# Kernel tuning notes

Hardware: AMD Instinct MI355X
Metric: run time of the kernel (lower is better)

## Reference

```python
import jax, jax.numpy as jnp
import numpy as np

N_ATOMS = 393216   # 4096 molecules * ~96 atoms
N_FEAT = 128
NB_FILTER = 128
NB_AFFINE = 11     # max_deg(10) + 1 - min_deg(0)
BATCH = 4096


def setup_inputs() -> dict:
    key = jax.random.key(0)
    k1, k2, k3, k4 = jax.random.split(key, 4)
    atoms = jax.random.normal(k1, (N_ATOMS, N_FEAT), jnp.float32)
    # stacked per-degree affine weights (glorot-ish scale)
    W = jax.random.normal(k2, (NB_AFFINE, N_FEAT, NB_FILTER), jnp.float32) / jnp.sqrt(jnp.float32(N_FEAT))
    b = jax.random.normal(k3, (NB_AFFINE, NB_FILTER), jnp.float32) * 0.01
    # contiguous degree layout: deg_slice[k] = (start, count), atoms sorted by degree
    counts = np.full(NB_AFFINE, N_ATOMS // NB_AFFINE, dtype=np.int32)
    counts[-1] += N_ATOMS - counts.sum()
    starts = np.concatenate([[0], np.cumsum(counts)[:-1]]).astype(np.int32)
    deg_slice = jnp.asarray(np.stack([starts, counts], axis=1))  # (11, 2) int32
    membership = jax.random.randint(k4, (N_ATOMS,), 0, BATCH, dtype=jnp.int32)
    return {"atoms": atoms, "W": W, "b": b, "deg_slice": deg_slice,
            "membership": membership, "batch_size": BATCH}


def reference(atoms, W, b, deg_slice, membership, batch_size):
    # atoms: (N, F); W: (K, F, O); b: (K, O); deg_slice: (K, 2)
    n = atoms.shape[0]
    nb_affine = W.shape[0]
    # Per-atom degree index from contiguous deg_slice layout:
    # deg_idx[i] = number of degree blocks that end at or before atom i.
    ends = jnp.cumsum(deg_slice[:, 1])                     # (K,)
    idx = jnp.arange(n, dtype=ends.dtype)
    deg_idx = jnp.sum(idx[:, None] >= ends[None, :], axis=1)  # (N,)
    # Per-degree affine: each atom uses the (W, b) of its degree block.
    out = jnp.zeros((n, W.shape[2]), dtype=atoms.dtype)
    for k in range(nb_affine):  # fixed small structural loop (11 distinct weight sets)
        yk = atoms @ W[k] + b[k]
        out = out + jnp.where((deg_idx == k)[:, None], yk, jnp.zeros((), atoms.dtype))
    # graph_gather: dynamic_partition + per-partition reduce_sum + concat == segment_sum
    pooled = jax.ops.segment_sum(out, membership, num_segments=batch_size)  # (B, O)
    # activation is 'linear' (identity); dropout is None
    return pooled
```

## Files before the change

### kernel.cpp

```cpp
#include <hip/hip_runtime.h>
#include <hip/hip_bf16.h>


typedef short bf16x8 __attribute__((ext_vector_type(8)));
typedef float f32x4  __attribute__((ext_vector_type(4)));

__device__ __forceinline__ unsigned short f2bf(float f) {
    unsigned int u = __builtin_bit_cast(unsigned int, f);
    u += 0x7fffu + ((u >> 16) & 1u);
    return (unsigned short)(u >> 16);
}

__device__ __forceinline__ int deg_of(int i, const int* __restrict__ ds, int K) {
    int k = 0, end = 0;
    for (int kk = 0; kk < K; ++kk) { end += ds[2 * kk + 1]; k += (i >= end) ? 1 : 0; }
    return k;
}

__global__ __launch_bounds__(256) void k_hist(
    const int* __restrict__ mem, const int* __restrict__ ds,
    unsigned* __restrict__ hist, int N, int K)
{
    int i = blockIdx.x * 256 + threadIdx.x;
    if (i >= N) return;
    int key = mem[i] * K + deg_of(i, ds, K);
    atomicAdd(&hist[key], 1u);
}

__global__ __launch_bounds__(1024) void k_scan(
    const unsigned* __restrict__ hist, unsigned* __restrict__ binstart, int B, int K)
{
    __shared__ unsigned segsum[4096];
    __shared__ unsigned aux[1024];
    int t = threadIdx.x;
    int CH = (B + 1023) >> 10;
    unsigned loc = 0;
    for (int j = 0; j < CH; ++j) {
        int s = t * CH + j;
        unsigned tot = 0;
        if (s < B) {
            for (int k = 0; k < K; ++k) tot += hist[s * K + k];
            segsum[s] = tot;
        }
        loc += tot;
    }
    aux[t] = loc;
    __syncthreads();
    for (int d = 1; d < 1024; d <<= 1) {
        unsigned v = (t >= d) ? aux[t - d] : 0u;
        __syncthreads();
        aux[t] += v;
        __syncthreads();
    }
    unsigned run = (t > 0) ? aux[t - 1] : 0u;
    for (int j = 0; j < CH; ++j) {
        int s = t * CH + j;
        if (s < B) {
            unsigned b2 = run;
            for (int k = 0; k < K; ++k) { binstart[s * K + k] = b2; b2 += hist[s * K + k]; }
            run = b2;
        }
    }
    if (t == 1023) binstart[(size_t)B * K] = run;
}

__global__ __launch_bounds__(256) void k_scatter(
    const int* __restrict__ mem, const int* __restrict__ ds,
    const unsigned* __restrict__ binstart, unsigned* __restrict__ cursor,
    unsigned* __restrict__ idx, int N, int K)
{
    int i = blockIdx.x * 256 + threadIdx.x;
    if (i >= N) return;
    int key = mem[i] * K + deg_of(i, ds, K);
    unsigned p = atomicAdd(&cursor[key], 1u);
    idx[binstart[key] + p] = (unsigned)i;
}

__global__ __launch_bounds__(256) void k_wconv(
    const float* __restrict__ W, unsigned short* __restrict__ Wb)
{
    __shared__ unsigned short t[128 * 130];
    int k = blockIdx.x;
    const float* Wk = W + (size_t)k * 16384;
    unsigned short* Wbk = Wb + (size_t)k * 16384;
    for (int e = threadIdx.x; e < 16384; e += 256) {
        int f = e >> 7, c = e & 127;
        t[f * 130 + c] = f2bf(Wk[e]);
    }
    __syncthreads();
    for (int e = threadIdx.x; e < 16384; e += 256) {
        int c = e >> 7, f = e & 127;
        Wbk[e] = t[f * 130 + c];
    }
}

__global__ __launch_bounds__(128) void k_phaseA(
    const float* __restrict__ atoms, const float* __restrict__ bias,
    const unsigned* __restrict__ binstart, const unsigned* __restrict__ idx,
    unsigned short* __restrict__ S, float* __restrict__ bsum, int K)
{
    int s = blockIdx.x, f = threadIdx.x;
    float bs = 0.f;
    for (int k = 0; k < K; ++k) {
        unsigned st = binstart[s * K + k];
        unsigned en = binstart[s * K + k + 1];
        float a0 = 0.f, a1 = 0.f, a2 = 0.f, a3 = 0.f;
        unsigned j = st;
        for (; j + 4 <= en; j += 4) {
            unsigned r0 = idx[j], r1 = idx[j + 1], r2 = idx[j + 2], r3 = idx[j + 3];
            a0 += atoms[(size_t)r0 * 128 + f];
            a1 += atoms[(size_t)r1 * 128 + f];
            a2 += atoms[(size_t)r2 * 128 + f];
            a3 += atoms[(size_t)r3 * 128 + f];
        }
        for (; j < en; ++j) a0 += atoms[(size_t)idx[j] * 128 + f];
        float acc = (a0 + a1) + (a2 + a3);
        S[(size_t)(s * K + k) * 128 + f] = f2bf(acc);
        bs += (float)(en - st) * bias[k * 128 + f];
    }
    bsum[(size_t)s * 128 + f] = bs;
}

__global__ __launch_bounds__(64) void k_phaseB(
    const unsigned short* __restrict__ S,
    const unsigned short* __restrict__ Wb,
    const float* __restrict__ bsum,
    float* __restrict__ out,
    int K)
{
    int bx   = blockIdx.x;
    int s0   = (bx >> 2) * 16;
    int c0   = (bx & 3) * 32;
    int lane = threadIdx.x;
    int quad = lane >> 4, cb = lane & 15;

    const int KD = K * 128;
    f32x4 acc0 = (f32x4){0.f, 0.f, 0.f, 0.f};
    f32x4 acc1 = (f32x4){0.f, 0.f, 0.f, 0.f};

    const unsigned short* Arow = S  + (size_t)(s0 + cb) * KD + quad * 8;
    const unsigned short* B0   = Wb + (size_t)(c0 + cb)      * 128 + quad * 8;
    const unsigned short* B1   = Wb + (size_t)(c0 + 16 + cb) * 128 + quad * 8;

    #pragma unroll 1
    for (int kk = 0; kk < K; ++kk) {
        #pragma unroll
        for (int k0 = 0; k0 < 128; k0 += 32) {
            bf16x8 a  = *reinterpret_cast<const bf16x8*>(Arow + kk * 128 + k0);
            bf16x8 b0 = *reinterpret_cast<const bf16x8*>(B0 + (size_t)kk * 16384 + k0);
            bf16x8 b1 = *reinterpret_cast<const bf16x8*>(B1 + (size_t)kk * 16384 + k0);
            acc0 = __builtin_amdgcn_mfma_f32_16x16x32_bf16(a, b0, acc0, 0, 0, 0);
            acc1 = __builtin_amdgcn_mfma_f32_16x16x32_bf16(a, b1, acc1, 0, 0, 0);
        }
    }
    #pragma unroll
    for (int reg = 0; reg < 4; ++reg) {
        int s = s0 + quad * 4 + reg;
        int c = c0 + cb;
        out[(size_t)s * 128 + c]      = acc0[reg] + bsum[(size_t)s * 128 + c];
        out[(size_t)s * 128 + c + 16] = acc1[reg] + bsum[(size_t)s * 128 + c + 16];
    }
}

#define TM 64
#define LDA 136
#define LDW 136
__global__ __launch_bounds__(256, 2) void degree_affine_pool(
    const float* __restrict__ atoms, const float* __restrict__ W,
    const float* __restrict__ bias, const int* __restrict__ deg_slice,
    const int* __restrict__ membership, float* __restrict__ out, int K)
{
    __shared__ unsigned short Alds[TM * LDA];
    __shared__ unsigned short Wlds[128 * LDW];
    const int bid = blockIdx.x, tid = threadIdx.x;
    int k = -1, tile = 0, acc_t = 0;
    for (int kk = 0; kk < K; ++kk) {
        int c = deg_slice[2 * kk + 1];
        int nt = (c + TM - 1) >> 6;
        if (k < 0 && bid < acc_t + nt) { k = kk; tile = bid - acc_t; }
        acc_t += nt;
    }
    if (k < 0) return;
    const int start = deg_slice[2 * k], cnt = deg_slice[2 * k + 1];
    const int row0 = start + tile * TM;
    const int rows_valid = min(TM, cnt - tile * TM);
    for (int e = tid; e < TM * 32; e += 256) {
        int r = e >> 5, f4 = e & 31;
        float4 v = make_float4(0.f, 0.f, 0.f, 0.f);
        if (r < rows_valid)
            v = *reinterpret_cast<const float4*>(atoms + (size_t)(row0 + r) * 128 + f4 * 4);
        unsigned lo = (unsigned)f2bf(v.x) | ((unsigned)f2bf(v.y) << 16);
        unsigned hi = (unsigned)f2bf(v.z) | ((unsigned)f2bf(v.w) << 16);
        *reinterpret_cast<uint2*>(&Alds[r * LDA + f4 * 4]) = make_uint2(lo, hi);
    }
    const float* Wk = W + (size_t)k * 16384;
    for (int e = tid; e < 8192; e += 256) {
        int c = e & 127, f2 = e >> 7;
        unsigned p = (unsigned)f2bf(Wk[(2 * f2) * 128 + c]) |
                     ((unsigned)f2bf(Wk[(2 * f2 + 1) * 128 + c]) << 16);
        *reinterpret_cast<unsigned*>(&Wlds[c * LDW + 2 * f2]) = p;
    }
    __syncthreads();
    const int wave = tid >> 6, lane = tid & 63, quad = lane >> 4, cb = lane & 15;
    f32x4 acc[8];
    #pragma unroll
    for (int ct = 0; ct < 8; ++ct) acc[ct] = (f32x4){0.f, 0.f, 0.f, 0.f};
    #pragma unroll
    for (int k0 = 0; k0 < 128; k0 += 32) {
        bf16x8 af = *reinterpret_cast<const bf16x8*>(&Alds[(wave * 16 + cb) * LDA + k0 + quad * 8]);
        #pragma unroll
        for (int ct = 0; ct < 8; ++ct) {
            bf16x8 bf = *reinterpret_cast<const bf16x8*>(&Wlds[(ct * 16 + cb) * LDW + k0 + quad * 8]);
            acc[ct] = __builtin_amdgcn_mfma_f32_16x16x32_bf16(af, bf, acc[ct], 0, 0, 0);
        }
    }
    int segs[4]; bool valid[4];
    #pragma unroll
    for (int reg = 0; reg < 4; ++reg) {
        int rl = wave * 16 + quad * 4 + reg;
        valid[reg] = (rl < rows_valid);
        segs[reg] = valid[reg] ? membership[row0 + rl] : 0;
    }
    const float* bk = bias + k * 128;
    #pragma unroll
    for (int ct = 0; ct < 8; ++ct) {
        int col = ct * 16 + cb;
        float bv = bk[col];
        #pragma unroll
        for (int reg = 0; reg < 4; ++reg)
            if (valid[reg])
                __hip_atomic_fetch_add(out + (size_t)segs[reg] * 128 + col,
                                       acc[ct][reg] + bv, __ATOMIC_RELAXED,
                                       __HIP_MEMORY_SCOPE_AGENT);
    }
}

static inline size_t aln(size_t x) { return (x + 255) & ~(size_t)255; }

extern "C" void kernel_launch(void* const* d_in, const int* in_sizes, int n_in,
                              void* d_out, int out_size, void* d_ws, size_t ws_size,
                              hipStream_t stream) {
    const float* atoms = (const float*)d_in[0];
    const float* W     = (const float*)d_in[1];
    const float* bias  = (const float*)d_in[2];
    const int*   deg   = (const int*)d_in[3];
    const int*   mem   = (const int*)d_in[4];
    float*       out   = (float*)d_out;

    const int K = in_sizes[3] / 2;
    const int N = in_sizes[0] / 128;
    const int B = out_size / 128;

    size_t oWb   = 0;                         size_t sWb   = (size_t)K * 16384 * 2;
    size_t oHist = aln(oWb + sWb);            size_t sHist = (size_t)B * K * 4;
    size_t oCur  = oHist + sHist;             size_t sCur  = sHist;
    size_t oBin  = aln(oCur + sCur);          size_t sBin  = ((size_t)B * K + 1) * 4;
    size_t oIdx  = aln(oBin + sBin);          size_t sIdx  = (size_t)N * 4;
    size_t oBsum = aln(oIdx + sIdx);          size_t sBsum = (size_t)B * 128 * 4;
    size_t oS    = aln(oBsum + sBsum);        size_t sS    = (size_t)B * K * 128 * 2;
    size_t total = oS + sS;

    if (ws_size < total || B > 4096) {
        (void)hipMemsetAsync(d_out, 0, (size_t)out_size * sizeof(float), stream);
        const int blocks = (N + TM - 1) / TM + K;
        degree_affine_pool<<<blocks, 256, 0, stream>>>(atoms, W, bias, deg, mem, out, K);
        return;
    }

    char* ws = (char*)d_ws;
    unsigned short* Wb   = (unsigned short*)(ws + oWb);
    unsigned*       hist = (unsigned*)(ws + oHist);
    unsigned*       cur  = (unsigned*)(ws + oCur);
    unsigned*       bin  = (unsigned*)(ws + oBin);
    unsigned*       idx  = (unsigned*)(ws + oIdx);
    float*          bsum = (float*)(ws + oBsum);
    unsigned short* S    = (unsigned short*)(ws + oS);

    (void)hipMemsetAsync(hist, 0, sHist + sCur, stream);

    const int nb = (N + 255) / 256;
    k_hist   <<<nb, 256, 0, stream>>>(mem, deg, hist, N, K);
    k_scan   <<<1, 1024, 0, stream>>>(hist, bin, B, K);
    k_scatter<<<nb, 256, 0, stream>>>(mem, deg, bin, cur, idx, N, K);
    k_wconv  <<<K, 256, 0, stream>>>(W, Wb);
    k_phaseA <<<B, 128, 0, stream>>>(atoms, bias, bin, idx, S, bsum, K);
    k_phaseB <<<(B / 16) * 4, 64, 0, stream>>>(S, Wb, bsum, out, K);
}
```

Baseline: 423.6 us.

## Fuse weight conversion into scan, drop cursor buffer, parallelize gather per bin

Merges the bf16 weight conversion into the scan launch as extra blocks, removing one kernel launch. The scatter now increments the bin start array directly, so after scatter it holds bin ends, which removes the separate cursor buffer and half of the memset. Phase A now gives each block two (segment, degree) bins instead of one segment with a serial loop over degrees, which exposes K times more blocks and uses 8-way unrolled gathers. The bias sum moves into the phase B epilogue, computed from bin counts. The trade-off is redundant bias loops in phase B and a tighter fallback condition.

```diff
diff --git a/kernel.cpp b/kernel.cpp
--- a/kernel.cpp
+++ b/kernel.cpp
@@ -27,22 +27,35 @@
     atomicAdd(&hist[key], 1u);
 }
 
-__global__ __launch_bounds__(1024) void k_scan(
-    const unsigned* __restrict__ hist, unsigned* __restrict__ binstart, int B, int K)
-{
-    __shared__ unsigned segsum[4096];
+__global__ __launch_bounds__(1024) void k_scan_wconv(
+    const unsigned* __restrict__ hist, unsigned* __restrict__ bin,
+    const float* __restrict__ W, unsigned short* __restrict__ Wb,
+    int B, int K)
+{
+    if ((int)blockIdx.x < K) {
+        __shared__ unsigned short t[128 * 130];
+        int k = blockIdx.x;
+        const float* Wk = W + (size_t)k * 16384;
+        unsigned short* Wbk = Wb + (size_t)k * 16384;
+        for (int e = threadIdx.x; e < 16384; e += 1024) {
+            int f = e >> 7, c = e & 127;
+            t[f * 130 + c] = f2bf(Wk[e]);
+        }
+        __syncthreads();
+        for (int e = threadIdx.x; e < 16384; e += 1024) {
+            int c = e >> 7, f = e & 127;
+            Wbk[e] = t[f * 130 + c];
+        }
+        return;
+    }
     __shared__ unsigned aux[1024];
     int t = threadIdx.x;
     int CH = (B + 1023) >> 10;
     unsigned loc = 0;
     for (int j = 0; j < CH; ++j) {
         int s = t * CH + j;
-        unsigned tot = 0;
-        if (s < B) {
-            for (int k = 0; k < K; ++k) tot += hist[s * K + k];
-            segsum[s] = tot;
-        }
-        loc += tot;
+        if (s < B)
+            for (int k = 0; k < K; ++k) loc += hist[s * K + k];
     }
     aux[t] = loc;
     __syncthreads();
@@ -56,75 +69,63 @@
     for (int j = 0; j < CH; ++j) {
         int s = t * CH + j;
         if (s < B) {
-            unsigned b2 = run;
-            for (int k = 0; k < K; ++k) { binstart[s * K + k] = b2; b2 += hist[s * K + k]; }
-            run = b2;
-        }
-    }
-    if (t == 1023) binstart[(size_t)B * K] = run;
+            for (int k = 0; k < K; ++k) { bin[s * K + k] = run; run += hist[s * K + k]; }
+        }
+    }
 }
 
 __global__ __launch_bounds__(256) void k_scatter(
     const int* __restrict__ mem, const int* __restrict__ ds,
-    const unsigned* __restrict__ binstart, unsigned* __restrict__ cursor,
-    unsigned* __restrict__ idx, int N, int K)
+    unsigned* __restrict__ bin, unsigned* __restrict__ idx, int N, int K)
 {
     int i = blockIdx.x * 256 + threadIdx.x;
     if (i >= N) return;
     int key = mem[i] * K + deg_of(i, ds, K);
-    unsigned p = atomicAdd(&cursor[key], 1u);
-    idx[binstart[key] + p] = (unsigned)i;
-}
-
-__global__ __launch_bounds__(256) void k_wconv(
-    const float* __restrict__ W, unsigned short* __restrict__ Wb)
-{
-    __shared__ unsigned short t[128 * 130];
-    int k = blockIdx.x;
-    const float* Wk = W + (size_t)k * 16384;
-    unsigned short* Wbk = Wb + (size_t)k * 16384;
-    for (int e = threadIdx.x; e < 16384; e += 256) {
-        int f = e >> 7, c = e & 127;
-        t[f * 130 + c] = f2bf(Wk[e]);
-    }
-    __syncthreads();
-    for (int e = threadIdx.x; e < 16384; e += 256) {
-        int c = e >> 7, f = e & 127;
-        Wbk[e] = t[f * 130 + c];
-    }
-}
-
-__global__ __launch_bounds__(128) void k_phaseA(
-    const float* __restrict__ atoms, const float* __restrict__ bias,
-    const unsigned* __restrict__ binstart, const unsigned* __restrict__ idx,
-    unsigned short* __restrict__ S, float* __restrict__ bsum, int K)
-{
-    int s = blockIdx.x, f = threadIdx.x;
-    float bs = 0.f;
-    for (int k = 0; k < K; ++k) {
-        unsigned st = binstart[s * K + k];
-        unsigned en = binstart[s * K + k + 1];
-        float a0 = 0.f, a1 = 0.f, a2 = 0.f, a3 = 0.f;
-        unsigned j = st;
-        for (; j + 4 <= en; j += 4) {
-            unsigned r0 = idx[j], r1 = idx[j + 1], r2 = idx[j + 2], r3 = idx[j + 3];
-            a0 += atoms[(size_t)r0 * 128 + f];
-            a1 += atoms[(size_t)r1 * 128 + f];
-            a2 += atoms[(size_t)r2 * 128 + f];
-            a3 += atoms[(size_t)r3 * 128 + f];
-        }
-        for (; j < en; ++j) a0 += atoms[(size_t)idx[j] * 128 + f];
-        float acc = (a0 + a1) + (a2 + a3);
-        S[(size_t)(s * K + k) * 128 + f] = f2bf(acc);
-        bs += (float)(en - st) * bias[k * 128 + f];
-    }
-    bsum[(size_t)s * 128 + f] = bs;
+    unsigned p = atomicAdd(&bin[key], 1u);
+    idx[p] = (unsigned)i;
+}
+
+__global__ __launch_bounds__(256) void k_phaseA(
+    const float* __restrict__ atoms,
+    const unsigned* __restrict__ binend,
+    const unsigned* __restrict__ idx,
+    unsigned short* __restrict__ S, int KB)
+{
+    int bin = blockIdx.x * 2 + (threadIdx.x >> 7);
+    int f   = threadIdx.x & 127;
+    if (bin >= KB) return;
+    unsigned st = (bin == 0) ? 0u : binend[bin - 1];
+    unsigned en = binend[bin];
+    float a0 = 0.f, a1 = 0.f, a2 = 0.f, a3 = 0.f;
+    float b0 = 0.f, b1 = 0.f, b2 = 0.f, b3 = 0.f;
+    unsigned j = st;
+    for (; j + 8 <= en; j += 8) {
+        unsigned r0 = idx[j+0], r1 = idx[j+1], r2 = idx[j+2], r3 = idx[j+3];
+        unsigned r4 = idx[j+4], r5 = idx[j+5], r6 = idx[j+6], r7 = idx[j+7];
+        a0 += atoms[(size_t)r0 * 128 + f]; a1 += atoms[(size_t)r1 * 128 + f];
+        a2 += atoms[(size_t)r2 * 128 + f]; a3 += atoms[(size_t)r3 * 128 + f];
+        b0 += atoms[(size_t)r4 * 128 + f]; b1 += atoms[(size_t)r5 * 128 + f];
+        b2 += atoms[(size_t)r6 * 128 + f]; b3 += atoms[(size_t)r7 * 128 + f];
+    }
+    if (j + 4 <= en) {
+        unsigned r0 = idx[j+0], r1 = idx[j+1], r2 = idx[j+2], r3 = idx[j+3];
+        a0 += atoms[(size_t)r0 * 128 + f]; a1 += atoms[(size_t)r1 * 128 + f];
+        a2 += atoms[(size_t)r2 * 128 + f]; a3 += atoms[(size_t)r3 * 128 + f];
+        j += 4;
+    }
+    unsigned rem = en - j;
+    if (rem > 0) b0 += atoms[(size_t)idx[j+0] * 128 + f];
+    if (rem > 1) b1 += atoms[(size_t)idx[j+1] * 128 + f];
+    if (rem > 2) b2 += atoms[(size_t)idx[j+2] * 128 + f];
+    float acc = ((a0 + a1) + (a2 + a3)) + ((b0 + b1) + (b2 + b3));
+    S[(size_t)bin * 128 + f] = f2bf(acc);
 }
 
 __global__ __launch_bounds__(64) void k_phaseB(
     const unsigned short* __restrict__ S,
     const unsigned short* __restrict__ Wb,
-    const float* __restrict__ bsum,
+    const unsigned* __restrict__ binend,
+    const float* __restrict__ bias,
     float* __restrict__ out,
     int K)
 {
@@ -156,9 +157,17 @@
     #pragma unroll
     for (int reg = 0; reg < 4; ++reg) {
         int s = s0 + quad * 4 + reg;
-        int c = c0 + cb;
-        out[(size_t)s * 128 + c]      = acc0[reg] + bsum[(size_t)s * 128 + c];
-        out[(size_t)s * 128 + c + 16] = acc1[reg] + bsum[(size_t)s * 128 + c + 16];
+        unsigned prev = (s == 0) ? 0u : binend[(size_t)s * K - 1];
+        float b0s = 0.f, b1s = 0.f;
+        for (int k = 0; k < K; ++k) {
+            unsigned e = binend[(size_t)s * K + k];
+            float cnt = (float)(e - prev);
+            prev = e;
+            b0s += cnt * bias[k * 128 + c0 + cb];
+            b1s += cnt * bias[k * 128 + c0 + 16 + cb];
+        }
+        out[(size_t)s * 128 + c0 + cb]      = acc0[reg] + b0s;
+        out[(size_t)s * 128 + c0 + 16 + cb] = acc1[reg] + b1s;
     }
 }
 
@@ -250,17 +259,16 @@
     const int K = in_sizes[3] / 2;
     const int N = in_sizes[0] / 128;
     const int B = out_size / 128;
+    const int KB = B * K;
 
     size_t oWb   = 0;                         size_t sWb   = (size_t)K * 16384 * 2;
-    size_t oHist = aln(oWb + sWb);            size_t sHist = (size_t)B * K * 4;
-    size_t oCur  = oHist + sHist;             size_t sCur  = sHist;
-    size_t oBin  = aln(oCur + sCur);          size_t sBin  = ((size_t)B * K + 1) * 4;
+    size_t oHist = aln(oWb + sWb);            size_t sHist = (size_t)KB * 4;
+    size_t oBin  = aln(oHist + sHist);        size_t sBin  = (size_t)KB * 4;
     size_t oIdx  = aln(oBin + sBin);          size_t sIdx  = (size_t)N * 4;
-    size_t oBsum = aln(oIdx + sIdx);          size_t sBsum = (size_t)B * 128 * 4;
-    size_t oS    = aln(oBsum + sBsum);        size_t sS    = (size_t)B * K * 128 * 2;
+    size_t oS    = aln(oIdx + sIdx);          size_t sS    = (size_t)KB * 128 * 2;
     size_t total = oS + sS;
 
-    if (ws_size < total || B > 4096) {
+    if (ws_size < total || (B & 15) != 0) {
         (void)hipMemsetAsync(d_out, 0, (size_t)out_size * sizeof(float), stream);
         const int blocks = (N + TM - 1) / TM + K;
         degree_affine_pool<<<blocks, 256, 0, stream>>>(atoms, W, bias, deg, mem, out, K);
@@ -270,19 +278,16 @@
     char* ws = (char*)d_ws;
     unsigned short* Wb   = (unsigned short*)(ws + oWb);
     unsigned*       hist = (unsigned*)(ws + oHist);
-    unsigned*       cur  = (unsigned*)(ws + oCur);
     unsigned*       bin  = (unsigned*)(ws + oBin);
     unsigned*       idx  = (unsigned*)(ws + oIdx);
-    float*          bsum = (float*)(ws + oBsum);
     unsigned short* S    = (unsigned short*)(ws + oS);
 
-    (void)hipMemsetAsync(hist, 0, sHist + sCur, stream);
+    (void)hipMemsetAsync(hist, 0, sHist, stream);
 
     const int nb = (N + 255) / 256;
-    k_hist   <<<nb, 256, 0, stream>>>(mem, deg, hist, N, K);
-    k_scan   <<<1, 1024, 0, stream>>>(hist, bin, B, K);
-    k_scatter<<<nb, 256, 0, stream>>>(mem, deg, bin, cur, idx, N, K);
-    k_wconv  <<<K, 256, 0, stream>>>(W, Wb);
-    k_phaseA <<<B, 128, 0, stream>>>(atoms, bias, bin, idx, S, bsum, K);
-    k_phaseB <<<(B / 16) * 4, 64, 0, stream>>>(S, Wb, bsum, out, K);
-}
+    k_hist      <<<nb, 256, 0, stream>>>(mem, deg, hist, N, K);
+    k_scan_wconv<<<K + 1, 1024, 0, stream>>>(hist, bin, W, Wb, B, K);
+    k_scatter   <<<nb, 256, 0, stream>>>(mem, deg, bin, idx, N, K);
+    k_phaseA    <<<(KB + 1) / 2, 256, 0, stream>>>(atoms, bin, idx, S, KB);
+    k_phaseB    <<<(B / 16) * 4, 64, 0, stream>>>(S, Wb, bin, bias, out, K);
+}
```

After: 428.5 us. About the same (+1.2%).
